# Kernel tuning notes

Measured on AMD Instinct MI355X. Metric: run time of the kernel, lower is better.

## Reference

```python
import jax, jax.numpy as jnp
import numpy as np

N, E, D, H, V = 50000, 800000, 64, 4, 10000

def setup_inputs() -> dict:
    key = jax.random.key(0)
    ks = jax.random.split(key, 12)
    inp = {
        'text_idx': jax.random.randint(ks[0], (N,), 0, V),
        'src': jax.random.randint(ks[1], (E,), 0, N),
        'dst': jax.random.randint(ks[2], (E,), 0, N),
        'emb': jax.random.normal(ks[3], (V, D), jnp.float32) * 0.02,
        'W_src': jax.random.normal(ks[4], (D, H * D), jnp.float32) / np.sqrt(D),
        'b_src': jnp.zeros((H * D,), jnp.float32),
        'W_dst': jax.random.normal(ks[5], (D, H * D), jnp.float32) / np.sqrt(D),
        'b_dst': jnp.zeros((H * D,), jnp.float32),
        'attn': jax.random.normal(ks[6], (H, D), jnp.float32) / np.sqrt(D),
        'W_res': jax.random.normal(ks[7], (D, H * D), jnp.float32) / np.sqrt(D),
        'Wg': jax.random.normal(ks[8], (D, D), jnp.float32) / np.sqrt(D),
        'bg': jnp.zeros((D,), jnp.float32),
    }
    return inp

def reference(text_idx, src, dst, emb, W_src, b_src, W_dst, b_dst, attn, W_res, Wg, bg):
    # --- node embedding ---
    h = emb[text_idx]                                   # [N, D]
    # --- layer 0: GATv2Conv (eval mode, dropout off), residual, ReLU ---
    fs = (h @ W_src + b_src).reshape(N, H, D)           # [N, H, D]
    fd = (h @ W_dst + b_dst).reshape(N, H, D)
    e = jax.nn.leaky_relu(fs[src] + fd[dst], 0.2)       # [E, H, D]
    logits = jnp.einsum('ehd,hd->eh', e, attn)          # [E, H]
    m = jax.ops.segment_max(logits, dst, num_segments=N)  # per-dst max
    a = jnp.exp(logits - m[dst])
    s = jax.ops.segment_sum(a, dst, num_segments=N)
    a = a / s[dst]                                      # edge softmax over incoming edges
    rst = jax.ops.segment_sum(a[:, :, None] * fs[src], dst, num_segments=N)  # [N, H, D]
    rst = rst + (h @ W_res).reshape(N, H, D)            # residual (in != H*out -> linear)
    h1 = jax.nn.relu(rst).mean(axis=1)                  # mean over heads -> [N, D]
    # --- layer 1: GraphConv(norm='both'), bias, ReLU ---
    ones = jnp.ones((E,), h1.dtype)
    out_deg = jnp.clip(jax.ops.segment_sum(ones, src, num_segments=N), 1.0)
    in_deg = jnp.clip(jax.ops.segment_sum(ones, dst, num_segments=N), 1.0)
    hh = (h1 * (out_deg ** -0.5)[:, None]) @ Wg         # [N, D]
    agg = jax.ops.segment_sum(hh[src], dst, num_segments=N)
    out = jax.nn.relu(agg * (in_deg ** -0.5)[:, None] + bg)
    return out
```

## Files before the change

kernel.cpp:

```cpp
#include <hip/hip_runtime.h>
#include <hip/hip_fp16.h>
#include <math.h>

#define D 64
#define H 4
#define HD 256
#define CAP 64

struct __align__(8)  half4 { __half2 h[2]; };
struct __align__(16) half8 { __half2 h[4]; };

typedef _Float16 f16x2 __attribute__((ext_vector_type(2)));

static __device__ __forceinline__ float fdot2(__half2 a, __half2 b, float c) {
#if __has_builtin(__builtin_amdgcn_fdot2)
    return __builtin_amdgcn_fdot2(__builtin_bit_cast(f16x2, a),
                                  __builtin_bit_cast(f16x2, b), c, false);
#else
    const float2 af = __half22float2(a), bf = __half22float2(b);
    return fmaf(af.x, bf.x, fmaf(af.y, bf.y, c));
#endif
}

static __device__ __forceinline__ __half2 lrelu2(__half2 x, __half2 c06, __half2 c04) {
    const unsigned ax = __builtin_bit_cast(unsigned, x) & 0x7FFF7FFFu;
    return __hfma2(__builtin_bit_cast(__half2, ax), c04, __hmul2(x, c06));
}

__global__ __launch_bounds__(256) void feat_hist_kernel(
    const float* __restrict__ emb,
    const float* __restrict__ W_src, const float* __restrict__ b_src,
    const float* __restrict__ W_dst, const float* __restrict__ b_dst,
    const float* __restrict__ W_res,
    __half* __restrict__ fsh, __half* __restrict__ fdh, float* __restrict__ fres_v,
    int V, int VB,
    const int* __restrict__ src, const int* __restrict__ dst,
    const int* __restrict__ text_idx, int E,
    int* __restrict__ deg_in, int* __restrict__ deg_out,
    int2* __restrict__ pair_pad)
{
    __shared__ float hT[16][D];
    const int tid = threadIdx.x;

    if (blockIdx.x >= VB) {
        const int e = (blockIdx.x - VB) * 256 + tid;
        if (e < E) {
            const int s = src[e];
            const int t = dst[e];
            const int r = atomicAdd(&deg_in[t], 1);
            atomicAdd(&deg_out[s], 1);
            if (r < CAP) pair_pad[(size_t)t * CAP + r] = make_int2(text_idx[s], s);
        }
        return;
    }

    const int base = blockIdx.x * 16;

    for (int i = tid; i < 16 * D; i += 256) {
        const int row = i >> 6, d = i & 63;
        hT[row][d] = (base + row < V) ? emb[(size_t)(base + row) * D + d] : 0.f;
    }
    __syncthreads();

    float as[16], ad[16], ar[16];
    const float bs = b_src[tid];
    const float bd = b_dst[tid];
#pragma unroll
    for (int i = 0; i < 16; ++i) { as[i] = bs; ad[i] = bd; ar[i] = 0.f; }

    for (int d = 0; d < D; ++d) {
        const float ws = W_src[d * HD + tid];
        const float wd = W_dst[d * HD + tid];
        const float wr = W_res[d * HD + tid];
#pragma unroll
        for (int i = 0; i < 16; ++i) {
            const float h = hT[i][d];
            as[i] = fmaf(h, ws, as[i]);
            ad[i] = fmaf(h, wd, ad[i]);
            ar[i] = fmaf(h, wr, ar[i]);
        }
    }
    const int nvalid = min(16, V - base);
    for (int i = 0; i < nvalid; ++i) {
        fsh   [(size_t)(base + i) * HD + tid] = __float2half(as[i]);
        fdh   [(size_t)(base + i) * HD + tid] = __float2half(ad[i]);
        fres_v[(size_t)(base + i) * HD + tid] = ar[i];
    }
}

__global__ __launch_bounds__(256) void gat_fused_wave2(
    const int2* __restrict__ pair_pad, const int* __restrict__ deg_in,
    const int* __restrict__ deg_out, const int* __restrict__ text_idx,
    const __half* __restrict__ fsh, const __half* __restrict__ fdh,
    const float* __restrict__ fres_v, const float* __restrict__ attn,
    float* __restrict__ h1, int N)
{
    const int n   = blockIdx.x * 8 + (threadIdx.x >> 5);
    const int sub = threadIdx.x & 31;
    if (n >= N) return;

    const int deg = min(deg_in[n], CAP);
    const int rs  = n * CAP;
    const int re  = rs + deg;
    const int tn  = text_idx[n];

    const half8 fdv = *(const half8*)(fdh + (size_t)tn * HD + sub * 8);
    const float4 atA = *(const float4*)(attn + sub * 8);
    const float4 atB = *(const float4*)(attn + sub * 8 + 4);
    const __half2 at0 = __floats2half2_rn(atA.x, atA.y);
    const __half2 at1 = __floats2half2_rn(atA.z, atA.w);
    const __half2 at2 = __floats2half2_rn(atB.x, atB.y);
    const __half2 at3 = __floats2half2_rn(atB.z, atB.w);
    const __half2 c06 = __floats2half2_rn(0.6f, 0.6f);
    const __half2 c04 = __floats2half2_rn(0.4f, 0.4f);
    const __half2 zero2 = __floats2half2_rn(0.f, 0.f);

    __half2 acc0 = zero2, acc1 = zero2, acc2 = zero2, acc3 = zero2;
    float wsum = 0.f;
    int k = rs;

#define EDGE_BODY(F, P)                                                        \
    float P = fdot2(lrelu2(__hadd2(F.h[3], fdv.h[3]), c06, c04), at3, 0.f);    \
    P       = fdot2(lrelu2(__hadd2(F.h[2], fdv.h[2]), c06, c04), at2, P);      \
    P       = fdot2(lrelu2(__hadd2(F.h[1], fdv.h[1]), c06, c04), at1, P);      \
    P       = fdot2(lrelu2(__hadd2(F.h[0], fdv.h[0]), c06, c04), at0, P);

#define ACC_BODY(F, W)                                                         \
    {                                                                          \
        const __half2 w2_ = __floats2half2_rn(W, W);                           \
        acc0 = __hfma2(w2_, F.h[0], acc0); acc1 = __hfma2(w2_, F.h[1], acc1);  \
        acc2 = __hfma2(w2_, F.h[2], acc2); acc3 = __hfma2(w2_, F.h[3], acc3);  \
    }

    for (; k + 4 <= re; k += 4) {
        const int t0 = pair_pad[k].x,     t1 = pair_pad[k + 1].x;
        const int t2 = pair_pad[k + 2].x, t3 = pair_pad[k + 3].x;
        const half8 f0 = *(const half8*)(fsh + (size_t)t0 * HD + sub * 8);
        const half8 f1 = *(const half8*)(fsh + (size_t)t1 * HD + sub * 8);
        const half8 f2 = *(const half8*)(fsh + (size_t)t2 * HD + sub * 8);
        const half8 f3 = *(const half8*)(fsh + (size_t)t3 * HD + sub * 8);

        EDGE_BODY(f0, p0) EDGE_BODY(f1, p1) EDGE_BODY(f2, p2) EDGE_BODY(f3, p3)

        p0 += __shfl_xor(p0, 1); p1 += __shfl_xor(p1, 1);
        p2 += __shfl_xor(p2, 1); p3 += __shfl_xor(p3, 1);
        p0 += __shfl_xor(p0, 2); p1 += __shfl_xor(p1, 2);
        p2 += __shfl_xor(p2, 2); p3 += __shfl_xor(p3, 2);
        p0 += __shfl_xor(p0, 4); p1 += __shfl_xor(p1, 4);
        p2 += __shfl_xor(p2, 4); p3 += __shfl_xor(p3, 4);

        const float w0 = __expf(p0), w1 = __expf(p1);
        const float w2 = __expf(p2), w3 = __expf(p3);
        wsum += (w0 + w1) + (w2 + w3);

        ACC_BODY(f0, w0) ACC_BODY(f1, w1) ACC_BODY(f2, w2) ACC_BODY(f3, w3)
    }
    for (; k < re; ++k) {
        const int t0 = pair_pad[k].x;
        const half8 f0 = *(const half8*)(fsh + (size_t)t0 * HD + sub * 8);
        EDGE_BODY(f0, p0)
        p0 += __shfl_xor(p0, 1);
        p0 += __shfl_xor(p0, 2);
        p0 += __shfl_xor(p0, 4);
        const float w0 = __expf(p0);
        wsum += w0;
        ACC_BODY(f0, w0)
    }
#undef EDGE_BODY
#undef ACC_BODY

    const float sinv = (deg > 0) ? 1.f / wsum : 0.f;

    float r[8];
    {
        const float2 t0 = __half22float2(acc0), t1 = __half22float2(acc1);
        const float2 t2 = __half22float2(acc2), t3 = __half22float2(acc3);
        r[0] = t0.x; r[1] = t0.y; r[2] = t1.x; r[3] = t1.y;
        r[4] = t2.x; r[5] = t2.y; r[6] = t3.x; r[7] = t3.y;
    }

    const float4 rv0 = *(const float4*)(fres_v + (size_t)tn * HD + sub * 8);
    const float4 rv1 = *(const float4*)(fres_v + (size_t)tn * HD + sub * 8 + 4);
    r[0] = fmaxf(fmaf(r[0], sinv, rv0.x), 0.f);
    r[1] = fmaxf(fmaf(r[1], sinv, rv0.y), 0.f);
    r[2] = fmaxf(fmaf(r[2], sinv, rv0.z), 0.f);
    r[3] = fmaxf(fmaf(r[3], sinv, rv0.w), 0.f);
    r[4] = fmaxf(fmaf(r[4], sinv, rv1.x), 0.f);
    r[5] = fmaxf(fmaf(r[5], sinv, rv1.y), 0.f);
    r[6] = fmaxf(fmaf(r[6], sinv, rv1.z), 0.f);
    r[7] = fmaxf(fmaf(r[7], sinv, rv1.w), 0.f);

#pragma unroll
    for (int i = 0; i < 8; ++i) {
        r[i] += __shfl_xor(r[i], 8);
        r[i] += __shfl_xor(r[i], 16);
    }

    const float sc = 0.25f / sqrtf((float)max(deg_out[n], 1));
    if (sub < 8) {
        float4 o0 = { r[0] * sc, r[1] * sc, r[2] * sc, r[3] * sc };
        float4 o1 = { r[4] * sc, r[5] * sc, r[6] * sc, r[7] * sc };
        *(float4*)(h1 + (size_t)n * D + sub * 8)     = o0;
        *(float4*)(h1 + (size_t)n * D + sub * 8 + 4) = o1;
    }
}

__global__ __launch_bounds__(256) void mm64_kernel(
    const float* __restrict__ h1, const float* __restrict__ Wg,
    __half* __restrict__ hh, int N)
{
    __shared__ float hT[64][D];
    const int base = blockIdx.x * 64;
    const int tid  = threadIdx.x;

    for (int i = tid; i < 64 * 16; i += 256) {
        const int r = i >> 4, c4 = (i & 15) * 4;
        float4 v = {0.f, 0.f, 0.f, 0.f};
        if (base + r < N) v = *(const float4*)(h1 + (size_t)(base + r) * D + c4);
        *(float4*)&hT[r][c4] = v;
    }
    __syncthreads();

    const int col = tid & 63;
    const int rg  = tid >> 6;
    float acc[16];
#pragma unroll
    for (int r = 0; r < 16; ++r) acc[r] = 0.f;

    for (int d = 0; d < D; ++d) {
        const float w = Wg[d * D + col];
#pragma unroll
        for (int r = 0; r < 16; ++r)
            acc[r] = fmaf(hT[rg * 16 + r][d], w, acc[r]);
    }
#pragma unroll
    for (int r = 0; r < 16; ++r) {
        const int node = base + rg * 16 + r;
        if (node < N) hh[(size_t)node * D + col] = __float2half(acc[r]);
    }
}

__global__ __launch_bounds__(256) void gconv_wave2(
    const int2* __restrict__ pair_pad, const int* __restrict__ deg_in,
    const __half* __restrict__ hh, const float* __restrict__ bg,
    float* __restrict__ out, int N)
{
    const int n   = blockIdx.x * 8 + (threadIdx.x >> 5);
    const int sub = threadIdx.x & 31;
    if (n >= N) return;

    const int deg = min(deg_in[n], CAP);
    const int rs  = n * CAP;
    const int re  = rs + deg;

    float ax = 0.f, ay = 0.f;
    int k = rs;
    for (; k + 4 <= re; k += 4) {
        const int s0 = pair_pad[k].y,     s1 = pair_pad[k + 1].y;
        const int s2 = pair_pad[k + 2].y, s3 = pair_pad[k + 3].y;
        const float2 v0 = __half22float2(*(const __half2*)(hh + (size_t)s0 * D + sub * 2));
        const float2 v1 = __half22float2(*(const __half2*)(hh + (size_t)s1 * D + sub * 2));
        const float2 v2 = __half22float2(*(const __half2*)(hh + (size_t)s2 * D + sub * 2));
        const float2 v3 = __half22float2(*(const __half2*)(hh + (size_t)s3 * D + sub * 2));
        ax += (v0.x + v1.x) + (v2.x + v3.x);
        ay += (v0.y + v1.y) + (v2.y + v3.y);
    }
    for (; k < re; ++k) {
        const float2 v = __half22float2(*(const __half2*)(hh + (size_t)pair_pad[k].y * D + sub * 2));
        ax += v.x; ay += v.y;
    }

    const float is = 1.f / sqrtf((float)max(deg, 1));
    const float2 b = *(const float2*)(bg + sub * 2);
    float2 o = { fmaxf(fmaf(ax, is, b.x), 0.f), fmaxf(fmaf(ay, is, b.y), 0.f) };
    *(float2*)(out + (size_t)n * D + sub * 2) = o;
}

extern "C" void kernel_launch(void* const* d_in, const int* in_sizes, int n_in,
                              void* d_out, int out_size, void* d_ws, size_t ws_size,
                              hipStream_t stream)
{
    const int*   text_idx = (const int*)  d_in[0];
    const int*   src      = (const int*)  d_in[1];
    const int*   dst      = (const int*)  d_in[2];
    const float* emb      = (const float*)d_in[3];
    const float* W_src    = (const float*)d_in[4];
    const float* b_src    = (const float*)d_in[5];
    const float* W_dst    = (const float*)d_in[6];
    const float* b_dst    = (const float*)d_in[7];
    const float* attn     = (const float*)d_in[8];
    const float* W_res    = (const float*)d_in[9];
    const float* Wg       = (const float*)d_in[10];
    const float* bg       = (const float*)d_in[11];

    const int N = in_sizes[0];
    const int E = in_sizes[1];
    const int V = in_sizes[3] / D;
    const int VB = (V + 15) / 16;
    const int EB = (E + 255) / 256;

    char* ws = (char*)d_ws;
    size_t off = 0;
    auto alloc = [&](size_t bytes) -> char* {
        char* p = ws + off;
        off = (off + bytes + 255) & ~(size_t)255;
        return p;
    };

    __half* fsh      = (__half*)alloc((size_t)V * HD * sizeof(__half));
    __half* fdh      = (__half*)alloc((size_t)V * HD * sizeof(__half));
    float*  fres_v   = (float*)alloc((size_t)V * HD * sizeof(float));
    float*  h1       = (float*)alloc((size_t)N * D * sizeof(float));
    __half* hh       = (__half*)alloc((size_t)N * D * sizeof(__half));
    int2*   pair_pad = (int2*) alloc((size_t)N * CAP * sizeof(int2));
    int*    deg      = (int*)  alloc((size_t)2 * N * sizeof(int));

    if (off > ws_size) return;

    int* deg_in  = deg;
    int* deg_out = deg + N;
    float* out = (float*)d_out;

    hipMemsetAsync(deg, 0, (size_t)2 * N * sizeof(int), stream);

    feat_hist_kernel<<<VB + EB, 256, 0, stream>>>(
        emb, W_src, b_src, W_dst, b_dst, W_res, fsh, fdh, fres_v, V, VB,
        src, dst, text_idx, E, deg_in, deg_out, pair_pad);

    gat_fused_wave2<<<(N + 7) / 8, 256, 0, stream>>>(
        pair_pad, deg_in, deg_out, text_idx, fsh, fdh, fres_v, attn, h1, N);

    mm64_kernel<<<(N + 63) / 64, 256, 0, stream>>>(h1, Wg, hh, N);

    gconv_wave2<<<(N + 7) / 8, 256, 0, stream>>>(pair_pad, deg_in, hh, bg, out, N);
}
```

Measured before the change: 179.9 us.

## Compute out-degree via packed LDS histograms and a merge pass

```diff
diff --git a/kernel.cpp b/kernel.cpp
--- a/kernel.cpp
+++ b/kernel.cpp
@@ -6,6 +6,8 @@
 #define H 4
 #define HD 256
 #define CAP 64
+#define NBH 256
+#define MAXW 12800
 
 struct __align__(8)  half4 { __half2 h[2]; };
 struct __align__(16) half8 { __half2 h[4]; };
@@ -25,6 +27,47 @@
 static __device__ __forceinline__ __half2 lrelu2(__half2 x, __half2 c06, __half2 c04) {
     const unsigned ax = __builtin_bit_cast(unsigned, x) & 0x7FFF7FFFu;
     return __hfma2(__builtin_bit_cast(__half2, ax), c04, __hmul2(x, c06));
+}
+
+__global__ __launch_bounds__(256) void degout_hist(
+    const int* __restrict__ src, int E, int NW,
+    unsigned* __restrict__ partial)
+{
+    __shared__ unsigned cnt[MAXW];
+    const int tid = threadIdx.x;
+    for (int i = tid; i < NW; i += 256) cnt[i] = 0u;
+    __syncthreads();
+
+    const int EPB = (E + NBH - 1) / NBH;
+    const int lo  = blockIdx.x * EPB;
+    const int hi  = min(lo + EPB, E);
+    for (int e = lo + tid; e < hi; e += 256) {
+        const int s = src[e];
+        atomicAdd(&cnt[s >> 2], 1u << (8 * (s & 3)));
+    }
+    __syncthreads();
+
+    unsigned* out = partial + (size_t)blockIdx.x * NW;
+    for (int i = tid; i < NW; i += 256) out[i] = cnt[i];
+}
+
+__global__ __launch_bounds__(256) void degout_merge(
+    const unsigned* __restrict__ partial, int NW, int N,
+    int* __restrict__ deg_out)
+{
+    const int j = blockIdx.x * 256 + threadIdx.x;
+    if (j >= NW) return;
+    unsigned a0 = 0, a1 = 0, a2 = 0, a3 = 0;
+    for (int b = 0; b < NBH; ++b) {
+        const unsigned w = partial[(size_t)b * NW + j];
+        a0 += w & 255u; a1 += (w >> 8) & 255u;
+        a2 += (w >> 16) & 255u; a3 += (w >> 24) & 255u;
+    }
+    const int n0 = j * 4;
+    if (n0     < N) deg_out[n0]     = (int)a0;
+    if (n0 + 1 < N) deg_out[n0 + 1] = (int)a1;
+    if (n0 + 2 < N) deg_out[n0 + 2] = (int)a2;
+    if (n0 + 3 < N) deg_out[n0 + 3] = (int)a3;
 }
 
 __global__ __launch_bounds__(256) void feat_hist_kernel(
@@ -36,7 +79,7 @@
     int V, int VB,
     const int* __restrict__ src, const int* __restrict__ dst,
     const int* __restrict__ text_idx, int E,
-    int* __restrict__ deg_in, int* __restrict__ deg_out,
+    int* __restrict__ deg_in, int* __restrict__ deg_out, int do_dout,
     int2* __restrict__ pair_pad)
 {
     __shared__ float hT[16][D];
@@ -48,7 +91,7 @@
             const int s = src[e];
             const int t = dst[e];
             const int r = atomicAdd(&deg_in[t], 1);
-            atomicAdd(&deg_out[s], 1);
+            if (do_dout) atomicAdd(&deg_out[s], 1);
             if (r < CAP) pair_pad[(size_t)t * CAP + r] = make_int2(text_idx[s], s);
         }
         return;
@@ -298,6 +341,8 @@
     const int V = in_sizes[3] / D;
     const int VB = (V + 15) / 16;
     const int EB = (E + 255) / 256;
+    const int NW = (N + 3) / 4;
+    const int use_lds_hist = (NW <= MAXW) ? 1 : 0;
 
     char* ws = (char*)d_ws;
     size_t off = 0;
@@ -307,13 +352,14 @@
         return p;
     };
 
-    __half* fsh      = (__half*)alloc((size_t)V * HD * sizeof(__half));
-    __half* fdh      = (__half*)alloc((size_t)V * HD * sizeof(__half));
-    float*  fres_v   = (float*)alloc((size_t)V * HD * sizeof(float));
-    float*  h1       = (float*)alloc((size_t)N * D * sizeof(float));
-    __half* hh       = (__half*)alloc((size_t)N * D * sizeof(__half));
-    int2*   pair_pad = (int2*) alloc((size_t)N * CAP * sizeof(int2));
-    int*    deg      = (int*)  alloc((size_t)2 * N * sizeof(int));
+    __half*   fsh      = (__half*)alloc((size_t)V * HD * sizeof(__half));
+    __half*   fdh      = (__half*)alloc((size_t)V * HD * sizeof(__half));
+    float*    fres_v   = (float*)alloc((size_t)V * HD * sizeof(float));
+    float*    h1       = (float*)alloc((size_t)N * D * sizeof(float));
+    __half*   hh       = (__half*)alloc((size_t)N * D * sizeof(__half));
+    int2*     pair_pad = (int2*) alloc((size_t)N * CAP * sizeof(int2));
+    int*      deg      = (int*)  alloc((size_t)2 * N * sizeof(int));
+    unsigned* partial  = (unsigned*)alloc((size_t)NBH * NW * sizeof(unsigned));
 
     if (off > ws_size) return;
 
@@ -321,11 +367,19 @@
     int* deg_out = deg + N;
     float* out = (float*)d_out;
 
-    hipMemsetAsync(deg, 0, (size_t)2 * N * sizeof(int), stream);
+    hipMemsetAsync(deg, 0, (size_t)(use_lds_hist ? N : 2 * N) * sizeof(int), stream);
+
+    if (use_lds_hist) {
+        degout_hist<<<NBH, 256, 0, stream>>>(src, E, NW, partial);
+    }
 
     feat_hist_kernel<<<VB + EB, 256, 0, stream>>>(
         emb, W_src, b_src, W_dst, b_dst, W_res, fsh, fdh, fres_v, V, VB,
-        src, dst, text_idx, E, deg_in, deg_out, pair_pad);
+        src, dst, text_idx, E, deg_in, deg_out, use_lds_hist ? 0 : 1, pair_pad);
+
+    if (use_lds_hist) {
+        degout_merge<<<(NW + 255) / 256, 256, 0, stream>>>(partial, NW, N, deg_out);
+    }
 
     gat_fused_wave2<<<(N + 7) / 8, 256, 0, stream>>>(
         pair_pad, deg_in, deg_out, text_idx, fsh, fdh, fres_v, attn, h1, N);
```

New measurement: 201.3 us. 11.9% more time.

## Move out-degree histogram into GAT kernel, store h1 in fp16, scale in matmul

Applied to the files above, without the earlier changes.

```diff
diff --git a/kernel.cpp b/kernel.cpp
--- a/kernel.cpp
+++ b/kernel.cpp
@@ -36,8 +36,7 @@
     int V, int VB,
     const int* __restrict__ src, const int* __restrict__ dst,
     const int* __restrict__ text_idx, int E,
-    int* __restrict__ deg_in, int* __restrict__ deg_out,
-    int2* __restrict__ pair_pad)
+    int* __restrict__ deg_in, int2* __restrict__ pair_pad)
 {
     __shared__ float hT[16][D];
     const int tid = threadIdx.x;
@@ -48,7 +47,6 @@
             const int s = src[e];
             const int t = dst[e];
             const int r = atomicAdd(&deg_in[t], 1);
-            atomicAdd(&deg_out[s], 1);
             if (r < CAP) pair_pad[(size_t)t * CAP + r] = make_int2(text_idx[s], s);
         }
         return;
@@ -90,12 +88,19 @@
 
 __global__ __launch_bounds__(256) void gat_fused_wave2(
     const int2* __restrict__ pair_pad, const int* __restrict__ deg_in,
-    const int* __restrict__ deg_out, const int* __restrict__ text_idx,
+    const int* __restrict__ text_idx,
     const __half* __restrict__ fsh, const __half* __restrict__ fdh,
     const float* __restrict__ fres_v, const float* __restrict__ attn,
-    float* __restrict__ h1, int N)
-{
-    const int n   = blockIdx.x * 8 + (threadIdx.x >> 5);
+    const int* __restrict__ src, int E, int EB, int* __restrict__ deg_out,
+    __half* __restrict__ h1h, int N)
+{
+    if (blockIdx.x < EB) {
+        const int e = blockIdx.x * 256 + threadIdx.x;
+        if (e < E) atomicAdd(&deg_out[src[e]], 1);
+        return;
+    }
+
+    const int n   = (blockIdx.x - EB) * 8 + (threadIdx.x >> 5);
     const int sub = threadIdx.x & 31;
     if (n >= N) return;
 
@@ -196,28 +201,38 @@
         r[i] += __shfl_xor(r[i], 16);
     }
 
-    const float sc = 0.25f / sqrtf((float)max(deg_out[n], 1));
     if (sub < 8) {
-        float4 o0 = { r[0] * sc, r[1] * sc, r[2] * sc, r[3] * sc };
-        float4 o1 = { r[4] * sc, r[5] * sc, r[6] * sc, r[7] * sc };
-        *(float4*)(h1 + (size_t)n * D + sub * 8)     = o0;
-        *(float4*)(h1 + (size_t)n * D + sub * 8 + 4) = o1;
+        half8 o;
+        o.h[0] = __floats2half2_rn(r[0], r[1]);
+        o.h[1] = __floats2half2_rn(r[2], r[3]);
+        o.h[2] = __floats2half2_rn(r[4], r[5]);
+        o.h[3] = __floats2half2_rn(r[6], r[7]);
+        *(half8*)(h1h + (size_t)n * D + sub * 8) = o;
     }
 }
 
 __global__ __launch_bounds__(256) void mm64_kernel(
-    const float* __restrict__ h1, const float* __restrict__ Wg,
+    const __half* __restrict__ h1h, const float* __restrict__ Wg,
+    const int* __restrict__ deg_out,
     __half* __restrict__ hh, int N)
 {
     __shared__ float hT[64][D];
     const int base = blockIdx.x * 64;
     const int tid  = threadIdx.x;
 
-    for (int i = tid; i < 64 * 16; i += 256) {
-        const int r = i >> 4, c4 = (i & 15) * 4;
-        float4 v = {0.f, 0.f, 0.f, 0.f};
-        if (base + r < N) v = *(const float4*)(h1 + (size_t)(base + r) * D + c4);
-        *(float4*)&hT[r][c4] = v;
+    for (int i = tid; i < 64 * 8; i += 256) {
+        const int r = i >> 3, c8 = (i & 7) * 8;
+        half8 v;
+        v.h[0] = v.h[1] = v.h[2] = v.h[3] = __floats2half2_rn(0.f, 0.f);
+        if (base + r < N) v = *(const half8*)(h1h + (size_t)(base + r) * D + c8);
+        const float2 f0 = __half22float2(v.h[0]);
+        const float2 f1 = __half22float2(v.h[1]);
+        const float2 f2 = __half22float2(v.h[2]);
+        const float2 f3 = __half22float2(v.h[3]);
+        hT[r][c8]     = f0.x; hT[r][c8 + 1] = f0.y;
+        hT[r][c8 + 2] = f1.x; hT[r][c8 + 3] = f1.y;
+        hT[r][c8 + 4] = f2.x; hT[r][c8 + 5] = f2.y;
+        hT[r][c8 + 6] = f3.x; hT[r][c8 + 7] = f3.y;
     }
     __syncthreads();
 
@@ -236,7 +251,10 @@
 #pragma unroll
     for (int r = 0; r < 16; ++r) {
         const int node = base + rg * 16 + r;
-        if (node < N) hh[(size_t)node * D + col] = __float2half(acc[r]);
+        if (node < N) {
+            const float sc = 0.25f / sqrtf((float)max(deg_out[node], 1));
+            hh[(size_t)node * D + col] = __float2half(acc[r] * sc);
+        }
     }
 }
 
@@ -255,15 +273,21 @@
 
     float ax = 0.f, ay = 0.f;
     int k = rs;
-    for (; k + 4 <= re; k += 4) {
+    for (; k + 8 <= re; k += 8) {
         const int s0 = pair_pad[k].y,     s1 = pair_pad[k + 1].y;
         const int s2 = pair_pad[k + 2].y, s3 = pair_pad[k + 3].y;
+        const int s4 = pair_pad[k + 4].y, s5 = pair_pad[k + 5].y;
+        const int s6 = pair_pad[k + 6].y, s7 = pair_pad[k + 7].y;
         const float2 v0 = __half22float2(*(const __half2*)(hh + (size_t)s0 * D + sub * 2));
         const float2 v1 = __half22float2(*(const __half2*)(hh + (size_t)s1 * D + sub * 2));
         const float2 v2 = __half22float2(*(const __half2*)(hh + (size_t)s2 * D + sub * 2));
         const float2 v3 = __half22float2(*(const __half2*)(hh + (size_t)s3 * D + sub * 2));
-        ax += (v0.x + v1.x) + (v2.x + v3.x);
-        ay += (v0.y + v1.y) + (v2.y + v3.y);
+        const float2 v4 = __half22float2(*(const __half2*)(hh + (size_t)s4 * D + sub * 2));
+        const float2 v5 = __half22float2(*(const __half2*)(hh + (size_t)s5 * D + sub * 2));
+        const float2 v6 = __half22float2(*(const __half2*)(hh + (size_t)s6 * D + sub * 2));
+        const float2 v7 = __half22float2(*(const __half2*)(hh + (size_t)s7 * D + sub * 2));
+        ax += ((v0.x + v1.x) + (v2.x + v3.x)) + ((v4.x + v5.x) + (v6.x + v7.x));
+        ay += ((v0.y + v1.y) + (v2.y + v3.y)) + ((v4.y + v5.y) + (v6.y + v7.y));
     }
     for (; k < re; ++k) {
         const float2 v = __half22float2(*(const __half2*)(hh + (size_t)pair_pad[k].y * D + sub * 2));
@@ -310,7 +334,7 @@
     __half* fsh      = (__half*)alloc((size_t)V * HD * sizeof(__half));
     __half* fdh      = (__half*)alloc((size_t)V * HD * sizeof(__half));
     float*  fres_v   = (float*)alloc((size_t)V * HD * sizeof(float));
-    float*  h1       = (float*)alloc((size_t)N * D * sizeof(float));
+    __half* h1h      = (__half*)alloc((size_t)N * D * sizeof(__half));
     __half* hh       = (__half*)alloc((size_t)N * D * sizeof(__half));
     int2*   pair_pad = (int2*) alloc((size_t)N * CAP * sizeof(int2));
     int*    deg      = (int*)  alloc((size_t)2 * N * sizeof(int));
@@ -325,12 +349,13 @@
 
     feat_hist_kernel<<<VB + EB, 256, 0, stream>>>(
         emb, W_src, b_src, W_dst, b_dst, W_res, fsh, fdh, fres_v, V, VB,
-        src, dst, text_idx, E, deg_in, deg_out, pair_pad);
-
-    gat_fused_wave2<<<(N + 7) / 8, 256, 0, stream>>>(
-        pair_pad, deg_in, deg_out, text_idx, fsh, fdh, fres_v, attn, h1, N);
-
-    mm64_kernel<<<(N + 63) / 64, 256, 0, stream>>>(h1, Wg, hh, N);
+        src, dst, text_idx, E, deg_in, pair_pad);
+
+    gat_fused_wave2<<<EB + (N + 7) / 8, 256, 0, stream>>>(
+        pair_pad, deg_in, text_idx, fsh, fdh, fres_v, attn,
+        src, E, EB, deg_out, h1h, N);
+
+    mm64_kernel<<<(N + 63) / 64, 256, 0, stream>>>(h1h, Wg, deg_out, hh, N);
 
     gconv_wave2<<<(N + 7) / 8, 256, 0, stream>>>(pair_pad, deg_in, hh, bg, out, N);
 }
```

After: 201.7 us. 12.1% more time.

## Fuse Wg matmul into graph-conv aggregation by reordering aggregate-then-multiply

Applied to the files above, without the earlier changes.

```diff
diff --git a/kernel.cpp b/kernel.cpp
--- a/kernel.cpp
+++ b/kernel.cpp
@@ -93,7 +93,7 @@
     const int* __restrict__ deg_out, const int* __restrict__ text_idx,
     const __half* __restrict__ fsh, const __half* __restrict__ fdh,
     const float* __restrict__ fres_v, const float* __restrict__ attn,
-    float* __restrict__ h1, int N)
+    __half* __restrict__ h1s, int N)
 {
     const int n   = blockIdx.x * 8 + (threadIdx.x >> 5);
     const int sub = threadIdx.x & 31;
@@ -198,82 +198,72 @@
 
     const float sc = 0.25f / sqrtf((float)max(deg_out[n], 1));
     if (sub < 8) {
-        float4 o0 = { r[0] * sc, r[1] * sc, r[2] * sc, r[3] * sc };
-        float4 o1 = { r[4] * sc, r[5] * sc, r[6] * sc, r[7] * sc };
-        *(float4*)(h1 + (size_t)n * D + sub * 8)     = o0;
-        *(float4*)(h1 + (size_t)n * D + sub * 8 + 4) = o1;
-    }
-}
-
-__global__ __launch_bounds__(256) void mm64_kernel(
-    const float* __restrict__ h1, const float* __restrict__ Wg,
-    __half* __restrict__ hh, int N)
-{
-    __shared__ float hT[64][D];
-    const int base = blockIdx.x * 64;
-    const int tid  = threadIdx.x;
-
-    for (int i = tid; i < 64 * 16; i += 256) {
-        const int r = i >> 4, c4 = (i & 15) * 4;
-        float4 v = {0.f, 0.f, 0.f, 0.f};
-        if (base + r < N) v = *(const float4*)(h1 + (size_t)(base + r) * D + c4);
-        *(float4*)&hT[r][c4] = v;
-    }
-    __syncthreads();
-
-    const int col = tid & 63;
-    const int rg  = tid >> 6;
-    float acc[16];
-#pragma unroll
-    for (int r = 0; r < 16; ++r) acc[r] = 0.f;
-
-    for (int d = 0; d < D; ++d) {
-        const float w = Wg[d * D + col];
-#pragma unroll
-        for (int r = 0; r < 16; ++r)
-            acc[r] = fmaf(hT[rg * 16 + r][d], w, acc[r]);
-    }
-#pragma unroll
-    for (int r = 0; r < 16; ++r) {
-        const int node = base + rg * 16 + r;
-        if (node < N) hh[(size_t)node * D + col] = __float2half(acc[r]);
-    }
-}
-
-__global__ __launch_bounds__(256) void gconv_wave2(
+        half8 o;
+        o.h[0] = __floats2half2_rn(r[0] * sc, r[1] * sc);
+        o.h[1] = __floats2half2_rn(r[2] * sc, r[3] * sc);
+        o.h[2] = __floats2half2_rn(r[4] * sc, r[5] * sc);
+        o.h[3] = __floats2half2_rn(r[6] * sc, r[7] * sc);
+        *(half8*)(h1s + (size_t)n * D + sub * 8) = o;
+    }
+}
+
+__global__ __launch_bounds__(256) void gconv_mm(
     const int2* __restrict__ pair_pad, const int* __restrict__ deg_in,
-    const __half* __restrict__ hh, const float* __restrict__ bg,
+    const __half* __restrict__ h1s, const float* __restrict__ Wg,
+    const float* __restrict__ bg,
     float* __restrict__ out, int N)
 {
-    const int n   = blockIdx.x * 8 + (threadIdx.x >> 5);
+    __shared__ float agg[8][D];
+    const int w   = threadIdx.x >> 5;
     const int sub = threadIdx.x & 31;
-    if (n >= N) return;
-
-    const int deg = min(deg_in[n], CAP);
-    const int rs  = n * CAP;
-    const int re  = rs + deg;
+    const int n   = blockIdx.x * 8 + w;
+    const bool valid = (n < N);
 
     float ax = 0.f, ay = 0.f;
-    int k = rs;
-    for (; k + 4 <= re; k += 4) {
-        const int s0 = pair_pad[k].y,     s1 = pair_pad[k + 1].y;
-        const int s2 = pair_pad[k + 2].y, s3 = pair_pad[k + 3].y;
-        const float2 v0 = __half22float2(*(const __half2*)(hh + (size_t)s0 * D + sub * 2));
-        const float2 v1 = __half22float2(*(const __half2*)(hh + (size_t)s1 * D + sub * 2));
-        const float2 v2 = __half22float2(*(const __half2*)(hh + (size_t)s2 * D + sub * 2));
-        const float2 v3 = __half22float2(*(const __half2*)(hh + (size_t)s3 * D + sub * 2));
-        ax += (v0.x + v1.x) + (v2.x + v3.x);
-        ay += (v0.y + v1.y) + (v2.y + v3.y);
-    }
-    for (; k < re; ++k) {
-        const float2 v = __half22float2(*(const __half2*)(hh + (size_t)pair_pad[k].y * D + sub * 2));
-        ax += v.x; ay += v.y;
-    }
-
-    const float is = 1.f / sqrtf((float)max(deg, 1));
-    const float2 b = *(const float2*)(bg + sub * 2);
-    float2 o = { fmaxf(fmaf(ax, is, b.x), 0.f), fmaxf(fmaf(ay, is, b.y), 0.f) };
-    *(float2*)(out + (size_t)n * D + sub * 2) = o;
+    int deg = 0;
+    if (valid) {
+        deg = min(deg_in[n], CAP);
+        const int rs = n * CAP;
+        const int re = rs + deg;
+        int k = rs;
+        for (; k + 8 <= re; k += 8) {
+            const int s0 = pair_pad[k].y,     s1 = pair_pad[k + 1].y;
+            const int s2 = pair_pad[k + 2].y, s3 = pair_pad[k + 3].y;
+            const int s4 = pair_pad[k + 4].y, s5 = pair_pad[k + 5].y;
+            const int s6 = pair_pad[k + 6].y, s7 = pair_pad[k + 7].y;
+            const float2 v0 = __half22float2(*(const __half2*)(h1s + (size_t)s0 * D + sub * 2));
+            const float2 v1 = __half22float2(*(const __half2*)(h1s + (size_t)s1 * D + sub * 2));
+            const float2 v2 = __half22float2(*(const __half2*)(h1s + (size_t)s2 * D + sub * 2));
+            const float2 v3 = __half22float2(*(const __half2*)(h1s + (size_t)s3 * D + sub * 2));
+            const float2 v4 = __half22float2(*(const __half2*)(h1s + (size_t)s4 * D + sub * 2));
+            const float2 v5 = __half22float2(*(const __half2*)(h1s + (size_t)s5 * D + sub * 2));
+            const float2 v6 = __half22float2(*(const __half2*)(h1s + (size_t)s6 * D + sub * 2));
+            const float2 v7 = __half22float2(*(const __half2*)(h1s + (size_t)s7 * D + sub * 2));
+            ax += ((v0.x + v1.x) + (v2.x + v3.x)) + ((v4.x + v5.x) + (v6.x + v7.x));
+            ay += ((v0.y + v1.y) + (v2.y + v3.y)) + ((v4.y + v5.y) + (v6.y + v7.y));
+        }
+        for (; k < re; ++k) {
+            const float2 v = __half22float2(*(const __half2*)(h1s + (size_t)pair_pad[k].y * D + sub * 2));
+            ax += v.x; ay += v.y;
+        }
+    }
+    agg[w][sub * 2]     = ax;
+    agg[w][sub * 2 + 1] = ay;
+    __syncthreads();
+
+    if (valid) {
+        float ox = 0.f, oy = 0.f;
+        for (int d = 0; d < D; ++d) {
+            const float a  = agg[w][d];
+            const float2 wv = *(const float2*)(Wg + d * D + sub * 2);
+            ox = fmaf(a, wv.x, ox);
+            oy = fmaf(a, wv.y, oy);
+        }
+        const float is = 1.f / sqrtf((float)max(deg, 1));
+        const float2 b = *(const float2*)(bg + sub * 2);
+        float2 o = { fmaxf(fmaf(ox, is, b.x), 0.f), fmaxf(fmaf(oy, is, b.y), 0.f) };
+        *(float2*)(out + (size_t)n * D + sub * 2) = o;
+    }
 }
 
 extern "C" void kernel_launch(void* const* d_in, const int* in_sizes, int n_in,
@@ -310,8 +300,7 @@
     __half* fsh      = (__half*)alloc((size_t)V * HD * sizeof(__half));
     __half* fdh      = (__half*)alloc((size_t)V * HD * sizeof(__half));
     float*  fres_v   = (float*)alloc((size_t)V * HD * sizeof(float));
-    float*  h1       = (float*)alloc((size_t)N * D * sizeof(float));
-    __half* hh       = (__half*)alloc((size_t)N * D * sizeof(__half));
+    __half* h1s      = (__half*)alloc((size_t)N * D * sizeof(__half));
     int2*   pair_pad = (int2*) alloc((size_t)N * CAP * sizeof(int2));
     int*    deg      = (int*)  alloc((size_t)2 * N * sizeof(int));
 
@@ -328,9 +317,8 @@
         src, dst, text_idx, E, deg_in, deg_out, pair_pad);
 
     gat_fused_wave2<<<(N + 7) / 8, 256, 0, stream>>>(
-        pair_pad, deg_in, deg_out, text_idx, fsh, fdh, fres_v, attn, h1, N);
-
-    mm64_kernel<<<(N + 63) / 64, 256, 0, stream>>>(h1, Wg, hh, N);
-
-    gconv_wave2<<<(N + 7) / 8, 256, 0, stream>>>(pair_pad, deg_in, hh, bg, out, N);
-}
+        pair_pad, deg_in, deg_out, text_idx, fsh, fdh, fres_v, attn, h1s, N);
+
+    gconv_mm<<<(N + 7) / 8, 256, 0, stream>>>(
+        pair_pad, deg_in, h1s, Wg, bg, out, N);
+}
```

Result: slower. 212.6 us (+18.2%).
